# Kernel optimization log

Measured on AMD Instinct MI355X. Metric: run time of the kernel, lower is better.

Reference implementation:

```python
import jax, jax.numpy as jnp
import numpy as np

EMBED_DIM = 1024
NUM_HEADS = 16
DEPTH = EMBED_DIM // NUM_HEADS  # 64
B, S = 4, 2048


def setup_inputs() -> dict:
    key = jax.random.key(0)
    ks = jax.random.split(key, 12)
    sc = 0.02
    return {
        "q": jax.random.normal(ks[0], (B, S, EMBED_DIM), jnp.float32),
        "k": jax.random.normal(ks[1], (B, S, EMBED_DIM), jnp.float32),
        "v": jax.random.normal(ks[2], (B, S, EMBED_DIM), jnp.float32),
        # per-head Dense(depth) weights stacked over heads: [H, D, depth]
        "wq": jax.random.normal(ks[3], (NUM_HEADS, EMBED_DIM, DEPTH), jnp.float32) * sc,
        "bq": jnp.zeros((NUM_HEADS, DEPTH), jnp.float32),
        "wk": jax.random.normal(ks[4], (NUM_HEADS, EMBED_DIM, DEPTH), jnp.float32) * sc,
        "bk": jnp.zeros((NUM_HEADS, DEPTH), jnp.float32),
        "wv": jax.random.normal(ks[5], (NUM_HEADS, EMBED_DIM, DEPTH), jnp.float32) * sc,
        "bv": jnp.zeros((NUM_HEADS, DEPTH), jnp.float32),
        # final Dense(embedding_dim): [D, D]
        "wo": jax.random.normal(ks[6], (EMBED_DIM, EMBED_DIM), jnp.float32) * sc,
        "bo": jnp.zeros((EMBED_DIM,), jnp.float32),
        "use_mask": 1,
    }


def reference(q, k, v, wq, bq, wk, bk, wv, bv, wo, bo, use_mask):
    # Batched per-head projections (equivalent to H separate Dense layers).
    qh = jnp.einsum('bsd,hde->bhse', q, wq) + bq[None, :, None, :]
    kh = jnp.einsum('bsd,hde->bhse', k, wk) + bk[None, :, None, :]
    vh = jnp.einsum('bsd,hde->bhse', v, wv) + bv[None, :, None, :]

    scale = 1.0 / jnp.sqrt(jnp.asarray(DEPTH, jnp.float32))
    logits = jnp.einsum('bhqe,bhke->bhqk', qh, kh) * scale  # [B,H,Sq,Sk]
    if use_mask:
        Sq, Sk = qh.shape[2], kh.shape[2]
        causal = jnp.triu(jnp.ones((Sq, Sk), jnp.float32), k=1)
        logits = logits + causal[None, None, :, :] * (-1e9)
    attn = jax.nn.softmax(logits, axis=-1)
    out_h = jnp.einsum('bhqk,bhke->bhqe', attn, vh)  # [B,H,Sq,depth]
    # concat heads along last dim -> [B,Sq,H*depth]
    bsz, H, Sq, dep = out_h.shape
    concat = out_h.transpose(0, 2, 1, 3).reshape(bsz, Sq, H * dep)
    return concat @ wo + bo
```

## Files before the change

kernel.cpp:

```cpp
#include <hip/hip_runtime.h>

#define B_ 4
#define S_ 2048
#define H_ 16
#define D_ 64
#define E_ 1024
#define M_ 8192

typedef __attribute__((ext_vector_type(8))) __bf16 bf16x8;
typedef __attribute__((ext_vector_type(4))) __bf16 bf16x4;
typedef __attribute__((ext_vector_type(4))) float f32x4;
typedef __attribute__((ext_vector_type(16))) float f32x16;

#define CEXPF (0.125f * 1.4426950408889634f)

__device__ __forceinline__ void gload_lds16(const void* g, void* l) {
  __builtin_amdgcn_global_load_lds(
      (const __attribute__((address_space(1))) unsigned int*)g,
      (__attribute__((address_space(3))) unsigned int*)l, 16, 0, 0);
}

__device__ __forceinline__ unsigned pk2(float a, float b) {
  union { __bf16 h; unsigned short u; } ua, ub;
  ua.h = (__bf16)a; ub.h = (__bf16)b;
  return ((unsigned)ub.u << 16) | (unsigned)ua.u;
}

__global__ void prep_all(const float* __restrict__ q, const float* __restrict__ k,
                         const float* __restrict__ v, const float* __restrict__ wq,
                         const float* __restrict__ wk, const float* __restrict__ wv,
                         const float* __restrict__ wo, __bf16* __restrict__ Aq,
                         __bf16* __restrict__ Ak, __bf16* __restrict__ Av,
                         __bf16* __restrict__ Bq, __bf16* __restrict__ Bk,
                         __bf16* __restrict__ Bv, __bf16* __restrict__ Bo) {
  const int y = blockIdx.y;
  if (y < 3) {
    const float* src = (y == 0) ? q : (y == 1) ? k : v;
    __bf16* dst = (y == 0) ? Aq : (y == 1) ? Ak : Av;
    const int i = blockIdx.x * blockDim.x + threadIdx.x;
    const float4 vv = ((const float4*)src)[i];
    bf16x4 o;
    o.x = (__bf16)vv.x; o.y = (__bf16)vv.y; o.z = (__bf16)vv.z; o.w = (__bf16)vv.w;
    ((bf16x4*)dst)[i] = o;
  } else {
    if (blockIdx.x >= 4096) return;
    const int yy = y - 3;
    const int idx = blockIdx.x * 256 + threadIdx.x;
    const int n = idx >> 10, kk = idx & 1023;
    if (yy < 3) {
      const float* w = (yy == 0) ? wq : (yy == 1) ? wk : wv;
      __bf16* out = (yy == 0) ? Bq : (yy == 1) ? Bk : Bv;
      out[idx] = (__bf16)w[((size_t)(n >> 6) << 16) + (kk << 6) + (n & 63)];
    } else {
      Bo[idx] = (__bf16)wo[((size_t)kk << 10) + n];
    }
  }
}

__global__ __launch_bounds__(256) void gemm_qk(
    const __bf16* __restrict__ Aq, const __bf16* __restrict__ Ak,
    const __bf16* __restrict__ Bq, const __bf16* __restrict__ Bk,
    const float* __restrict__ bq, const float* __restrict__ bk,
    __bf16* __restrict__ qhb, __bf16* __restrict__ khb) {
  constexpr int K = 1024;
  __shared__ __bf16 As[128 * 64];
  __shared__ __bf16 Bs[128 * 64];
  const int t = threadIdx.x;
  const int w = t >> 6, l = t & 63;
  const int isK = blockIdx.y >> 3;
  const __bf16* A = isK ? Ak : Aq;
  const __bf16* Bt = isK ? Bk : Bq;
  const float* bias = isK ? bk : bq;
  __bf16* C = isK ? khb : qhb;
  const int m0 = blockIdx.x * 128, n0 = (blockIdx.y & 7) * 128;
  f32x4 acc[4][4] = {};

  for (int kt = 0; kt < K / 64; ++kt) {
    const int kb = kt * 64;
#pragma unroll
    for (int j = 0; j < 4; ++j) {
      const int ci = (j * 4 + w) * 64 + l;
      const int row = ci >> 3;
      const int c = (ci & 7) ^ (row & 7);
      gload_lds16(A + (size_t)(m0 + row) * K + kb + c * 8, As + (j * 4 + w) * 512);
      gload_lds16(Bt + (size_t)(n0 + row) * K + kb + c * 8, Bs + (j * 4 + w) * 512);
    }
    __syncthreads();
#pragma unroll
    for (int kk = 0; kk < 64; kk += 32) {
      bf16x8 af[4], bfr[4];
#pragma unroll
      for (int f = 0; f < 4; ++f) {
        const int ra = (w >> 1) * 64 + f * 16 + (l & 15);
        const int ca = ((kk >> 3) + (l >> 4)) ^ (ra & 7);
        af[f] = *(const bf16x8*)(As + ra * 64 + ca * 8);
        const int rb = (w & 1) * 64 + f * 16 + (l & 15);
        const int cb = ((kk >> 3) + (l >> 4)) ^ (rb & 7);
        bfr[f] = *(const bf16x8*)(Bs + rb * 64 + cb * 8);
      }
#pragma unroll
      for (int mf = 0; mf < 4; ++mf)
#pragma unroll
        for (int nf = 0; nf < 4; ++nf)
          acc[mf][nf] = __builtin_amdgcn_mfma_f32_16x16x32_bf16(af[mf], bfr[nf],
                                                                acc[mf][nf], 0, 0, 0);
    }
    __syncthreads();
  }

#pragma unroll
  for (int mf = 0; mf < 4; ++mf)
#pragma unroll
    for (int nf = 0; nf < 4; ++nf)
#pragma unroll
      for (int r = 0; r < 4; ++r) {
        const int gm = m0 + (w >> 1) * 64 + mf * 16 + (l >> 4) * 4 + r;
        const int gn = n0 + (w & 1) * 64 + nf * 16 + (l & 15);
        const float val = acc[mf][nf][r] + bias[gn];
        C[(((size_t)(gm >> 11) * H_ + (gn >> 6)) * S_ + (gm & 2047)) * D_ + (gn & 63)] =
            (__bf16)val;
      }
}

template <int MODE>
__global__ __launch_bounds__(256) void gemm_bt(const __bf16* __restrict__ A,
                                               const __bf16* __restrict__ Bt,
                                               const float* __restrict__ bias,
                                               void* __restrict__ Cout) {
  constexpr int K = 1024;
  __shared__ __bf16 As[128 * 64];
  __shared__ __bf16 Bs[128 * 64];
  const int t = threadIdx.x;
  const int w = t >> 6, l = t & 63;
  const int m0 = blockIdx.x * 128, n0 = blockIdx.y * 128;
  f32x4 acc[4][4] = {};

  for (int kt = 0; kt < K / 64; ++kt) {
    const int kb = kt * 64;
#pragma unroll
    for (int j = 0; j < 4; ++j) {
      const int ci = (j * 4 + w) * 64 + l;
      const int row = ci >> 3;
      const int c = (ci & 7) ^ (row & 7);
      gload_lds16(A + (size_t)(m0 + row) * K + kb + c * 8, As + (j * 4 + w) * 512);
      gload_lds16(Bt + (size_t)(n0 + row) * K + kb + c * 8, Bs + (j * 4 + w) * 512);
    }
    __syncthreads();
#pragma unroll
    for (int kk = 0; kk < 64; kk += 32) {
      bf16x8 af[4], bfr[4];
#pragma unroll
      for (int f = 0; f < 4; ++f) {
        const int ra = (w >> 1) * 64 + f * 16 + (l & 15);
        const int ca = ((kk >> 3) + (l >> 4)) ^ (ra & 7);
        af[f] = *(const bf16x8*)(As + ra * 64 + ca * 8);
        const int rb = (w & 1) * 64 + f * 16 + (l & 15);
        const int cb = ((kk >> 3) + (l >> 4)) ^ (rb & 7);
        bfr[f] = *(const bf16x8*)(Bs + rb * 64 + cb * 8);
      }
#pragma unroll
      for (int mf = 0; mf < 4; ++mf)
#pragma unroll
        for (int nf = 0; nf < 4; ++nf)
          acc[mf][nf] = __builtin_amdgcn_mfma_f32_16x16x32_bf16(af[mf], bfr[nf],
                                                                acc[mf][nf], 0, 0, 0);
    }
    __syncthreads();
  }

#pragma unroll
  for (int mf = 0; mf < 4; ++mf) {
#pragma unroll
    for (int nf = 0; nf < 4; ++nf) {
#pragma unroll
      for (int r = 0; r < 4; ++r) {
        const int gm = m0 + (w >> 1) * 64 + mf * 16 + (l >> 4) * 4 + r;
        const int gn = n0 + (w & 1) * 64 + nf * 16 + (l & 15);
        const float val = acc[mf][nf][r] + ((MODE == 1) ? bias[gm] : bias[gn]);
        if constexpr (MODE == 1) {
          ((__bf16*)Cout)[(((size_t)(gn >> 11) * H_ + (gm >> 6)) * D_ + (gm & 63)) * S_ + (gn & 2047)] =
              (__bf16)val;
        } else {
          ((float*)Cout)[(size_t)gm * 1024 + gn] = val;
        }
      }
    }
  }
}

__device__ __forceinline__ void stage_k128(const __bf16* __restrict__ Kb, int kt,
                                           __bf16* Kdst, int t, int w) {
#pragma unroll
  for (int j = 0; j < 4; ++j) {
    const int ci = j * 256 + t;
    const int row = ci >> 3;
    const int sc = (ci & 7) ^ (row & 7);
    gload_lds16(Kb + (size_t)(kt * 128 + row) * D_ + sc * 8, Kdst + j * 2048 + w * 512);
  }
}
__device__ __forceinline__ void stage_v64(const __bf16* __restrict__ Vb, int col0,
                                          __bf16* Vdst, int t, int w) {
#pragma unroll
  for (int j = 0; j < 2; ++j) {
    const int ci = j * 256 + t;
    const int row = ci >> 3;
    const int sc = (ci & 7) ^ (row & 7);
    gload_lds16(Vb + (size_t)row * S_ + col0 + sc * 8, Vdst + j * 2048 + w * 512);
  }
}

__device__ __forceinline__ void attn_subtile(const __bf16* __restrict__ Ksub,
                                             const __bf16* __restrict__ Vsub,
                                             const bf16x8* qf, const bf16x8 ones,
                                             int lo, int hi, int qloc, bool diag,
                                             float& m, f32x16& lsacc,
                                             f32x16& o0, f32x16& o1) {
  f32x16 s0 = {}, s1 = {};
  __builtin_amdgcn_s_setprio(1);
#pragma unroll
  for (int ks = 0; ks < 4; ++ks) {
    const int ch = ((ks << 1) | hi) ^ (lo & 7);
    const bf16x8 k0 = *(const bf16x8*)(Ksub + lo * 64 + ch * 8);
    const bf16x8 k1 = *(const bf16x8*)(Ksub + (32 + lo) * 64 + ch * 8);
    s0 = __builtin_amdgcn_mfma_f32_32x32x16_bf16(k0, qf[ks], s0, 0, 0, 0);
    s1 = __builtin_amdgcn_mfma_f32_32x32x16_bf16(k1, qf[ks], s1, 0, 0, 0);
  }
  __builtin_amdgcn_s_setprio(0);

  if (diag) {
#pragma unroll
    for (int r = 0; r < 16; ++r) {
      const int kv0 = (r & 3) + 8 * (r >> 2) + 4 * hi;
      if (kv0 > qloc) s0[r] = -1e30f;
      if (kv0 + 32 > qloc) s1[r] = -1e30f;
    }
  }

  float pm = s0[0];
#pragma unroll
  for (int r = 1; r < 16; ++r) pm = fmaxf(pm, s0[r]);
#pragma unroll
  for (int r = 0; r < 16; ++r) pm = fmaxf(pm, s1[r]);

  if (!__all(pm - m <= 64.0f)) {
    const float pmp = fmaxf(pm, __shfl_xor(pm, 32));
    const float mn = fmaxf(m, pmp);
    const float al = __builtin_amdgcn_exp2f((m - mn) * CEXPF);
    m = mn;
    lsacc[0] *= al;
    o0 *= al;
    o1 *= al;
  }
  const float mneg = -m * CEXPF;

  unsigned W0[4][2], W1[4][2];
#pragma unroll
  for (int j = 0; j < 4; ++j) {
    float p0 = __builtin_amdgcn_exp2f(__builtin_fmaf(s0[4 * j + 0], CEXPF, mneg));
    float p1 = __builtin_amdgcn_exp2f(__builtin_fmaf(s0[4 * j + 1], CEXPF, mneg));
    float p2 = __builtin_amdgcn_exp2f(__builtin_fmaf(s0[4 * j + 2], CEXPF, mneg));
    float p3 = __builtin_amdgcn_exp2f(__builtin_fmaf(s0[4 * j + 3], CEXPF, mneg));
    W0[j][0] = pk2(p0, p1);
    W0[j][1] = pk2(p2, p3);
    float q0 = __builtin_amdgcn_exp2f(__builtin_fmaf(s1[4 * j + 0], CEXPF, mneg));
    float q1 = __builtin_amdgcn_exp2f(__builtin_fmaf(s1[4 * j + 1], CEXPF, mneg));
    float q2 = __builtin_amdgcn_exp2f(__builtin_fmaf(s1[4 * j + 2], CEXPF, mneg));
    float q3 = __builtin_amdgcn_exp2f(__builtin_fmaf(s1[4 * j + 3], CEXPF, mneg));
    W1[j][0] = pk2(q0, q1);
    W1[j][1] = pk2(q2, q3);
  }

  bf16x8 pa[4];
#pragma unroll
  for (int ks = 0; ks < 4; ++ks) {
    const int c = ks & 1;
    unsigned x0, x1, y0, y1;
    if ((ks >> 1) == 0) {
      x0 = W0[2 * c][0]; x1 = W0[2 * c][1];
      y0 = W0[2 * c + 1][0]; y1 = W0[2 * c + 1][1];
    } else {
      x0 = W1[2 * c][0]; x1 = W1[2 * c][1];
      y0 = W1[2 * c + 1][0]; y1 = W1[2 * c + 1][1];
    }
    asm volatile("v_permlane32_swap_b32 %0, %1" : "+v"(x0), "+v"(y0));
    asm volatile("v_permlane32_swap_b32 %0, %1" : "+v"(x1), "+v"(y1));
    union { unsigned u[4]; bf16x8 v; } uu;
    uu.u[0] = x0; uu.u[1] = x1; uu.u[2] = y0; uu.u[3] = y1;
    pa[ks] = uu.v;
  }

  __builtin_amdgcn_s_setprio(1);
#pragma unroll
  for (int ks = 0; ks < 4; ++ks) {
    const int ch = ((ks << 1) | hi) ^ (lo & 7);
    const bf16x8 v0 = *(const bf16x8*)(Vsub + lo * 64 + ch * 8);
    const bf16x8 v1 = *(const bf16x8*)(Vsub + (32 + lo) * 64 + ch * 8);
    o0 = __builtin_amdgcn_mfma_f32_32x32x16_bf16(v0, pa[ks], o0, 0, 0, 0);
    o1 = __builtin_amdgcn_mfma_f32_32x32x16_bf16(v1, pa[ks], o1, 0, 0, 0);
    lsacc = __builtin_amdgcn_mfma_f32_32x32x16_bf16(ones, pa[ks], lsacc, 0, 0, 0);
  }
  __builtin_amdgcn_s_setprio(0);
}

__global__ __launch_bounds__(256, 2) void attn_fused(const __bf16* __restrict__ qh,
                                                     const __bf16* __restrict__ kh,
                                                     const __bf16* __restrict__ vT,
                                                     __bf16* __restrict__ concat,
                                                     const int* __restrict__ use_mask_p) {
  __shared__ __bf16 Ks[2][128 * 64];
  __shared__ __bf16 Vs[2][2][64 * 64];
  const int t = threadIdx.x, w = t >> 6, l = t & 63;
  const int lo = l & 31, hi = l >> 5;
  const int bh = blockIdx.x, pr = blockIdx.y;
  const int usemask = *use_mask_p;
  const __bf16* Qb = qh + (size_t)bh * S_ * D_;
  const __bf16* Kb = kh + (size_t)bh * S_ * D_;
  const __bf16* Vb = vT + (size_t)bh * D_ * S_;
  const int b = bh >> 4, hh = bh & 15;
  const int qloc = ((w & 1) << 5) + lo;

  bf16x8 ones;
#pragma unroll
  for (int i = 0; i < 8; ++i) ones[i] = (__bf16)1.0f;

  const int qtA = pr, qtB = 15 - pr;
  const int qrow0A = qtA * 128 + w * 32, qrow0B = qtB * 128 + w * 32;
  const int nkt = usemask ? (qtB + 1) : (S_ / 128);
  const int ktwA = usemask ? (2 * qtA + (w >> 1)) : (1 << 30);
  const int ktwB = usemask ? (2 * qtB + (w >> 1)) : (1 << 30);

  bf16x8 qfA[4], qfB[4];
#pragma unroll
  for (int ks = 0; ks < 4; ++ks) {
    qfA[ks] = *(const bf16x8*)(Qb + (size_t)(qrow0A + lo) * D_ + ks * 16 + hi * 8);
    qfB[ks] = *(const bf16x8*)(Qb + (size_t)(qrow0B + lo) * D_ + ks * 16 + hi * 8);
  }

  float mA = -3e38f, mB = -3e38f;
  f32x16 lsA = {}, lsB = {};
  f32x16 oA0 = {}, oA1 = {}, oB0 = {}, oB1 = {};

  int cur = 0;
  stage_k128(Kb, 0, &Ks[0][0], t, w);
  stage_v64(Vb, 0, &Vs[0][0][0], t, w);
  stage_v64(Vb, 64, &Vs[0][1][0], t, w);

  for (int kt = 0; kt < nkt; ++kt) {
    __builtin_amdgcn_sched_barrier(0);
    asm volatile("s_waitcnt vmcnt(0)" ::: "memory");
    __builtin_amdgcn_s_barrier();
    __builtin_amdgcn_sched_barrier(0);

    if (kt + 1 < nkt) {
      const int nxt = cur ^ 1;
      stage_k128(Kb, kt + 1, &Ks[nxt][0], t, w);
      stage_v64(Vb, (kt + 1) * 128, &Vs[nxt][0][0], t, w);
      stage_v64(Vb, (kt + 1) * 128 + 64, &Vs[nxt][1][0], t, w);
    }

#pragma unroll
    for (int sub = 0; sub < 2; ++sub) {
      const int st = 2 * kt + sub;
      const __bf16* Ksub = &Ks[cur][sub * 64 * 64];
      const __bf16* Vsub = &Vs[cur][sub][0];
      if (st <= ktwA)
        attn_subtile(Ksub, Vsub, qfA, ones, lo, hi, qloc,
                     usemask && st == ktwA, mA, lsA, oA0, oA1);
      if (st <= ktwB)
        attn_subtile(Ksub, Vsub, qfB, ones, lo, hi, qloc,
                     usemask && st == ktwB, mB, lsB, oB0, oB1);
    }
    cur ^= 1;
  }

  {
    const float invA = 1.0f / lsA[0], invB = 1.0f / lsB[0];
    const size_t rbA = ((size_t)(b * S_ + qrow0A + lo)) * E_ + hh * 64;
    const size_t rbB = ((size_t)(b * S_ + qrow0B + lo)) * E_ + hh * 64;
#pragma unroll
    for (int rr = 0; rr < 4; ++rr) {
      bf16x4 a0, a1, b0, b1;
#pragma unroll
      for (int bb = 0; bb < 4; ++bb) {
        a0[bb] = (__bf16)(oA0[4 * rr + bb] * invA);
        a1[bb] = (__bf16)(oA1[4 * rr + bb] * invA);
        b0[bb] = (__bf16)(oB0[4 * rr + bb] * invB);
        b1[bb] = (__bf16)(oB1[4 * rr + bb] * invB);
      }
      *(bf16x4*)(concat + rbA + 8 * rr + 4 * hi) = a0;
      *(bf16x4*)(concat + rbA + 32 + 8 * rr + 4 * hi) = a1;
      *(bf16x4*)(concat + rbB + 8 * rr + 4 * hi) = b0;
      *(bf16x4*)(concat + rbB + 32 + 8 * rr + 4 * hi) = b1;
    }
  }
}

extern "C" void kernel_launch(void* const* d_in, const int* in_sizes, int n_in,
                              void* d_out, int out_size, void* d_ws, size_t ws_size,
                              hipStream_t stream) {
  const float* q = (const float*)d_in[0];
  const float* k = (const float*)d_in[1];
  const float* v = (const float*)d_in[2];
  const float* wq = (const float*)d_in[3];
  const float* bq = (const float*)d_in[4];
  const float* wk = (const float*)d_in[5];
  const float* bk = (const float*)d_in[6];
  const float* wv = (const float*)d_in[7];
  const float* bv = (const float*)d_in[8];
  const float* wo = (const float*)d_in[9];
  const float* bo = (const float*)d_in[10];
  const int* use_mask = (const int*)d_in[11];
  (void)in_sizes; (void)n_in; (void)out_size; (void)ws_size;

  char* ws = (char*)d_ws;
  __bf16* Aq = (__bf16*)ws;
  __bf16* Ak = Aq + (size_t)M_ * E_;
  __bf16* Av = Ak + (size_t)M_ * E_;
  __bf16* Bq = Av + (size_t)M_ * E_;
  __bf16* Bk = Bq + (size_t)E_ * E_;
  __bf16* Bv = Bk + (size_t)E_ * E_;
  __bf16* Bo = Bv + (size_t)E_ * E_;
  __bf16* qhb = Bo + (size_t)E_ * E_;
  __bf16* khb = qhb + (size_t)8388608;
  __bf16* vTb = khb + (size_t)8388608;
  __bf16* concat = Aq;

  prep_all<<<dim3(8192, 7), 256, 0, stream>>>(q, k, v, wq, wk, wv, wo,
                                              Aq, Ak, Av, Bq, Bk, Bv, Bo);
  gemm_qk<<<dim3(64, 16), 256, 0, stream>>>(Aq, Ak, Bq, Bk, bq, bk, qhb, khb);
  gemm_bt<1><<<dim3(8, 64), 256, 0, stream>>>(Bv, Av, bv, vTb);
  attn_fused<<<dim3(64, 8), 256, 0, stream>>>(qhb, khb, vTb, concat, use_mask);
  gemm_bt<2><<<dim3(64, 8), 256, 0, stream>>>(concat, Bo, bo, d_out);
}
```

Baseline: 194.4 us.

## Double-buffer LDS in projection GEMMs with K-step 32 and async prefetch

After: 223.3 us. 1.15x slower.

```diff
diff --git a/kernel.cpp b/kernel.cpp
--- a/kernel.cpp
+++ b/kernel.cpp
@@ -57,14 +57,57 @@
   }
 }
 
+#define F_ROW(r) ((((r) & 3)) ^ (((r) >> 2) & 3))
+
+#define GEMM32_STAGE(A_, Bt_, kt_, buf_)                                      \
+  {                                                                           \
+    const int kb_ = (kt_) * 32;                                               \
+    _Pragma("unroll") for (int j = 0; j < 2; ++j) {                           \
+      const int ci = (j * 4 + w) * 64 + l;                                    \
+      const int row = ci >> 2;                                                \
+      const int c = (ci & 3) ^ F_ROW(row);                                    \
+      gload_lds16((A_) + (size_t)(m0 + row) * 1024 + kb_ + c * 8,             \
+                  As[buf_] + (j * 4 + w) * 512);                              \
+      gload_lds16((Bt_) + (size_t)(n0 + row) * 1024 + kb_ + c * 8,            \
+                  Bs[buf_] + (j * 4 + w) * 512);                              \
+    }                                                                         \
+  }
+
+#define GEMM32_COMPUTE(buf_)                                                  \
+  {                                                                           \
+    bf16x8 af[4], bfr[4];                                                     \
+    _Pragma("unroll") for (int f = 0; f < 4; ++f) {                           \
+      const int ra = (w >> 1) * 64 + f * 16 + (l & 15);                       \
+      af[f] = *(const bf16x8*)(As[buf_] + ra * 32 + ((l >> 4) ^ F_ROW(ra)) * 8); \
+      const int rb = (w & 1) * 64 + f * 16 + (l & 15);                        \
+      bfr[f] = *(const bf16x8*)(Bs[buf_] + rb * 32 + ((l >> 4) ^ F_ROW(rb)) * 8); \
+    }                                                                         \
+    _Pragma("unroll") for (int mf = 0; mf < 4; ++mf)                          \
+      _Pragma("unroll") for (int nf = 0; nf < 4; ++nf)                        \
+        acc[mf][nf] = __builtin_amdgcn_mfma_f32_16x16x32_bf16(                \
+            af[mf], bfr[nf], acc[mf][nf], 0, 0, 0);                           \
+  }
+
+#define GEMM32_PIPE(A_, Bt_)                                                  \
+  GEMM32_STAGE(A_, Bt_, 0, 0);                                                \
+  int cur = 0;                                                                \
+  for (int kt = 0; kt < 32; ++kt) {                                           \
+    __builtin_amdgcn_sched_barrier(0);                                        \
+    asm volatile("s_waitcnt vmcnt(0)" ::: "memory");                          \
+    __builtin_amdgcn_s_barrier();                                             \
+    __builtin_amdgcn_sched_barrier(0);                                        \
+    if (kt + 1 < 32) GEMM32_STAGE(A_, Bt_, kt + 1, cur ^ 1);                  \
+    GEMM32_COMPUTE(cur);                                                      \
+    cur ^= 1;                                                                 \
+  }
+
 __global__ __launch_bounds__(256) void gemm_qk(
     const __bf16* __restrict__ Aq, const __bf16* __restrict__ Ak,
     const __bf16* __restrict__ Bq, const __bf16* __restrict__ Bk,
     const float* __restrict__ bq, const float* __restrict__ bk,
     __bf16* __restrict__ qhb, __bf16* __restrict__ khb) {
-  constexpr int K = 1024;
-  __shared__ __bf16 As[128 * 64];
-  __shared__ __bf16 Bs[128 * 64];
+  __shared__ __bf16 As[2][128 * 32];
+  __shared__ __bf16 Bs[2][128 * 32];
   const int t = threadIdx.x;
   const int w = t >> 6, l = t & 63;
   const int isK = blockIdx.y >> 3;
@@ -75,38 +118,7 @@
   const int m0 = blockIdx.x * 128, n0 = (blockIdx.y & 7) * 128;
   f32x4 acc[4][4] = {};
 
-  for (int kt = 0; kt < K / 64; ++kt) {
-    const int kb = kt * 64;
-#pragma unroll
-    for (int j = 0; j < 4; ++j) {
-      const int ci = (j * 4 + w) * 64 + l;
-      const int row = ci >> 3;
-      const int c = (ci & 7) ^ (row & 7);
-      gload_lds16(A + (size_t)(m0 + row) * K + kb + c * 8, As + (j * 4 + w) * 512);
-      gload_lds16(Bt + (size_t)(n0 + row) * K + kb + c * 8, Bs + (j * 4 + w) * 512);
-    }
-    __syncthreads();
-#pragma unroll
-    for (int kk = 0; kk < 64; kk += 32) {
-      bf16x8 af[4], bfr[4];
-#pragma unroll
-      for (int f = 0; f < 4; ++f) {
-        const int ra = (w >> 1) * 64 + f * 16 + (l & 15);
-        const int ca = ((kk >> 3) + (l >> 4)) ^ (ra & 7);
-        af[f] = *(const bf16x8*)(As + ra * 64 + ca * 8);
-        const int rb = (w & 1) * 64 + f * 16 + (l & 15);
-        const int cb = ((kk >> 3) + (l >> 4)) ^ (rb & 7);
-        bfr[f] = *(const bf16x8*)(Bs + rb * 64 + cb * 8);
-      }
-#pragma unroll
-      for (int mf = 0; mf < 4; ++mf)
-#pragma unroll
-        for (int nf = 0; nf < 4; ++nf)
-          acc[mf][nf] = __builtin_amdgcn_mfma_f32_16x16x32_bf16(af[mf], bfr[nf],
-                                                                acc[mf][nf], 0, 0, 0);
-    }
-    __syncthreads();
-  }
+  GEMM32_PIPE(A, Bt);
 
 #pragma unroll
   for (int mf = 0; mf < 4; ++mf)
@@ -127,46 +139,14 @@
                                                const __bf16* __restrict__ Bt,
                                                const float* __restrict__ bias,
                                                void* __restrict__ Cout) {
-  constexpr int K = 1024;
-  __shared__ __bf16 As[128 * 64];
-  __shared__ __bf16 Bs[128 * 64];
+  __shared__ __bf16 As[2][128 * 32];
+  __shared__ __bf16 Bs[2][128 * 32];
   const int t = threadIdx.x;
   const int w = t >> 6, l = t & 63;
   const int m0 = blockIdx.x * 128, n0 = blockIdx.y * 128;
   f32x4 acc[4][4] = {};
 
-  for (int kt = 0; kt < K / 64; ++kt) {
-    const int kb = kt * 64;
-#pragma unroll
-    for (int j = 0; j < 4; ++j) {
-      const int ci = (j * 4 + w) * 64 + l;
-      const int row = ci >> 3;
-      const int c = (ci & 7) ^ (row & 7);
-      gload_lds16(A + (size_t)(m0 + row) * K + kb + c * 8, As + (j * 4 + w) * 512);
-      gload_lds16(Bt + (size_t)(n0 + row) * K + kb + c * 8, Bs + (j * 4 + w) * 512);
-    }
-    __syncthreads();
-#pragma unroll
-    for (int kk = 0; kk < 64; kk += 32) {
-      bf16x8 af[4], bfr[4];
-#pragma unroll
-      for (int f = 0; f < 4; ++f) {
-        const int ra = (w >> 1) * 64 + f * 16 + (l & 15);
-        const int ca = ((kk >> 3) + (l >> 4)) ^ (ra & 7);
-        af[f] = *(const bf16x8*)(As + ra * 64 + ca * 8);
-        const int rb = (w & 1) * 64 + f * 16 + (l & 15);
-        const int cb = ((kk >> 3) + (l >> 4)) ^ (rb & 7);
-        bfr[f] = *(const bf16x8*)(Bs + rb * 64 + cb * 8);
-      }
-#pragma unroll
-      for (int mf = 0; mf < 4; ++mf)
-#pragma unroll
-        for (int nf = 0; nf < 4; ++nf)
-          acc[mf][nf] = __builtin_amdgcn_mfma_f32_16x16x32_bf16(af[mf], bfr[nf],
-                                                                acc[mf][nf], 0, 0, 0);
-    }
-    __syncthreads();
-  }
+  GEMM32_PIPE(A, Bt);
 
 #pragma unroll
   for (int mf = 0; mf < 4; ++mf) {
```
